# Kernel tuning notes

Hardware: AMD Instinct MI355X
Metric: run time of the kernel (lower is better)

## Reference

```python
import jax, jax.numpy as jnp
import numpy as np

NG, NT, E = 2500, 20000, 640000
SRC_DIM, DST_DIM, HID, OUT, NCLS = 128, 500, 128, 128, 16


def setup_inputs() -> dict:
    key = jax.random.key(0)
    ks = jax.random.split(key, 11)
    d = {
        "gene_feats": jax.random.normal(ks[0], (NG, SRC_DIM), jnp.float32),
        "train_feats": jax.random.normal(ks[1], (NT, DST_DIM), jnp.float32),
        "edge_src": jax.random.randint(ks[2], (E,), 0, NG),
        "edge_dst": jax.random.randint(ks[3], (E,), 0, NT),
        # conv1: SAGEConv((src_dim, dst_dim) -> hidden)
        "W1_neigh": jax.random.normal(ks[4], (SRC_DIM, HID), jnp.float32) / np.sqrt(SRC_DIM),
        "W1_self": jax.random.normal(ks[5], (DST_DIM, HID), jnp.float32) / np.sqrt(DST_DIM),
        "b1": jnp.zeros((HID,), jnp.float32),
        # conv2: SAGEConv(hidden -> out); src input is the raw gene features
        "W2_neigh": jax.random.normal(ks[6], (HID, OUT), jnp.float32) / np.sqrt(HID),
        "W2_self": jax.random.normal(ks[7], (HID, OUT), jnp.float32) / np.sqrt(HID),
        "b2": jnp.zeros((OUT,), jnp.float32),
        # classifier MLP
        "Wc1": jax.random.normal(ks[8], (OUT, OUT), jnp.float32) / np.sqrt(OUT),
        "bc1": jnp.zeros((OUT,), jnp.float32),
        "Wc2": jax.random.normal(ks[9], (OUT, NCLS), jnp.float32) / np.sqrt(OUT),
        "bc2": jnp.zeros((NCLS,), jnp.float32),
    }
    return d


def _segment_mean(msgs, dst, num_segments):
    # mean over in-edges; isolated dst nodes get 0 (DGL convention)
    sums = jax.ops.segment_sum(msgs, dst, num_segments=num_segments)
    cnt = jax.ops.segment_sum(jnp.ones((msgs.shape[0],), msgs.dtype), dst,
                              num_segments=num_segments)
    return sums / jnp.maximum(cnt, 1.0)[:, None]


def reference(gene_feats, train_feats, edge_src, edge_dst,
              W1_neigh, W1_self, b1, W2_neigh, W2_self, b2,
              Wc1, bc1, Wc2, bc2):
    # mean-aggregate gene (src) features onto train (dst) nodes
    agg = _segment_mean(gene_feats[edge_src], edge_dst, NT)  # [NT, SRC_DIM]
    # conv1: fc_self(h_dst) + fc_neigh(mean_neigh) + bias, then ReLU
    h1 = jax.nn.relu(train_feats @ W1_self + agg @ W1_neigh + b1)  # [NT, HID]
    # conv2 reuses raw gene features as src -> same mean aggregation
    h2 = jax.nn.relu(h1 @ W2_self + agg @ W2_neigh + b2)  # [NT, OUT]
    # classifier: Linear -> ReLU -> Linear
    return jax.nn.relu(h2 @ Wc1 + bc1) @ Wc2 + bc2  # [NT, NCLS]
```

## Files before the change

### kernel.cpp

```cpp
#include <hip/hip_runtime.h>


#define NG 2500
#define NT 20000
#define NE 640000
#define NCLS 16
#define CAP8 40
#define NTILE 1250

typedef unsigned short u16;
typedef unsigned int u32;

typedef float f32x4 __attribute__((ext_vector_type(4)));
typedef __bf16 bf16x8 __attribute__((ext_vector_type(8)));

__device__ __forceinline__ float b2f(u16 u) { return __uint_as_float(((u32)u) << 16); }
__device__ __forceinline__ float blo(u32 p) { return __uint_as_float(p << 16); }
__device__ __forceinline__ float bhi(u32 p) { return __uint_as_float(p & 0xffff0000u); }
__device__ __forceinline__ u16 f2b(float f) {
    u32 u = __float_as_uint(f);
    return (u16)((u + 0x7fffu + ((u >> 16) & 1u)) >> 16);
}

#define B1N 81920
#define B2N 32768
#define B3N 16384
#define B4N 2048
#define NEB 2500
#define CVB NTILE
#define GNB 625
#define PKB 520

__global__ __launch_bounds__(256) void k_prep(
    const int* __restrict__ esrc, const int* __restrict__ edst,
    int* __restrict__ cnt8, u16* __restrict__ csr8,
    const float* __restrict__ train, const float* __restrict__ gene,
    u16* __restrict__ AF, u32* __restrict__ GH32,
    const float* __restrict__ W1n, const float* __restrict__ W1s,
    const float* __restrict__ W2n, const float* __restrict__ W2s,
    const float* __restrict__ Wc1, const float* __restrict__ Wc2,
    u16* __restrict__ B1h, u16* __restrict__ B1l,
    u16* __restrict__ B2h, u16* __restrict__ B2l,
    u16* __restrict__ B3h, u16* __restrict__ B3l,
    u16* __restrict__ B4h, u16* __restrict__ B4l) {
    int blk = blockIdx.x, t = threadIdx.x;
    if (blk < NEB) {
        int xcc = __builtin_amdgcn_s_getreg(63508) & 7;
        int* mycnt = cnt8 + (size_t)xcc * NT;
        u16* mycsr = csr8 + (size_t)xcc * NT * CAP8;
        int e = blk * 256 + t;
        if (e < NE) {
            unsigned d = (unsigned)edst[e];
            if (d < NT) {
                int slot = atomicAdd(&mycnt[d], 1);
                if (slot < CAP8) mycsr[(size_t)d * CAP8 + slot] = (u16)esrc[e];
            }
        }
        return;
    }
    if (blk < NEB + CVB) {
        __shared__ __align__(16) u16 L[16 * 520];
        u32* L32 = (u32*)L;
        int tile = blk - NEB;
        for (int i = t; i < 160; i += 256) {
            int r = i / 10, c = i - r * 10;
            L32[r * 260 + 250 + c] = 0;
        }
        for (int i = t; i < 2000; i += 256) {
            int r = i / 125, c4 = i - r * 125;
            float4 v = *(const float4*)(train + (size_t)(tile * 16 + r) * 500 + c4 * 4);
            int base = r * 260 + c4 * 2;
            L32[base] = (u32)f2b(v.x) | ((u32)f2b(v.y) << 16);
            L32[base + 1] = (u32)f2b(v.z) | ((u32)f2b(v.w) << 16);
        }
        __syncthreads();
#pragma unroll
        for (int it = 0; it < 4; ++it) {
            int slot = t + it * 256;
            int kk = slot >> 6, lane = slot & 63;
            int m = lane & 15, q = lane >> 4;
            uint4 v = *(const uint4*)(L + m * 520 + kk * 32 + q * 8);
            *(uint4*)(AF + (((size_t)tile * 16 + kk) * 64 + lane) * 8) = v;
        }
        return;
    }
    if (blk < NEB + CVB + GNB) {
        int idx = (blk - NEB - CVB) * 256 + t;
        float2 v = ((const float2*)gene)[idx];
        GH32[idx] = (u32)f2b(v.x) | ((u32)f2b(v.y) << 16);
        return;
    }
    int idx = (blk - NEB - CVB - GNB) * 256 + t;
    float v = 0.f;
    u16 *ph = 0, *pl = 0;
    int off = 0;
    if (idx < B1N) {
        int j = idx & 7, l = (idx >> 3) & 63, rest = idx >> 9;
        int g = rest & 7, kk = rest >> 3;
        int k = kk * 32 + ((l >> 4) << 3) + j, n = (g << 4) + (l & 15);
        if (k < 500) v = W1s[k * 128 + n];
        else if (k >= 512) v = W1n[(k - 512) * 128 + n];
        ph = B1h; pl = B1l; off = idx;
    } else if (idx < B1N + B2N) {
        int e = idx - B1N;
        int j = e & 7, l = (e >> 3) & 63, rest = e >> 9;
        int g = rest & 7, kk = rest >> 3;
        int k = kk * 32 + ((l >> 4) << 3) + j, n = (g << 4) + (l & 15);
        v = (k < 128) ? W2s[k * 128 + n] : W2n[(k - 128) * 128 + n];
        ph = B2h; pl = B2l; off = e;
    } else if (idx < B1N + B2N + B3N) {
        int e = idx - (B1N + B2N);
        int j = e & 7, l = (e >> 3) & 63, rest = e >> 9;
        int g = rest & 7, kk = rest >> 3;
        int k = kk * 32 + ((l >> 4) << 3) + j, n = (g << 4) + (l & 15);
        v = Wc1[k * 128 + n];
        ph = B3h; pl = B3l; off = e;
    } else if (idx < B1N + B2N + B3N + B4N) {
        int e = idx - (B1N + B2N + B3N);
        int j = e & 7, l = (e >> 3) & 63, kk = e >> 9;
        int k = kk * 32 + ((l >> 4) << 3) + j, n = l & 15;
        v = Wc2[k * 16 + n];
        ph = B4h; pl = B4l; off = e;
    }
    if (ph) {
        u16 hi = f2b(v);
        u16 lo = f2b(v - b2f(hi));
        ph[off] = hi;
        pl[off] = lo;
    }
}

__global__ __launch_bounds__(512) void k_mega(
    const int* __restrict__ cnt8, const u16* __restrict__ csr8,
    const u16* __restrict__ GH, const u16* __restrict__ AF,
    const u16* __restrict__ B1h, const u16* __restrict__ B1l,
    const u16* __restrict__ B2h, const u16* __restrict__ B2l,
    const u16* __restrict__ B3h, const u16* __restrict__ B3l,
    const u16* __restrict__ B4h, const u16* __restrict__ B4l,
    const float* __restrict__ b1, const float* __restrict__ b2,
    const float* __restrict__ bc1, const float* __restrict__ bc2,
    float* __restrict__ out) {
    __shared__ __align__(16) u16 SAGh[32 * 136];
    __shared__ __align__(16) u16 S1h[32 * 136];
    __shared__ __align__(16) u16 S2h[32 * 136];
    int t = threadIdx.x;
    int row0 = blockIdx.x * 32;

    {
        int r = t >> 4, cg = t & 15;
        int d = row0 + r;
        float a[8];
#pragma unroll
        for (int p = 0; p < 8; ++p) a[p] = 0.f;
        int ctot = 0;
#pragma unroll
        for (int x = 0; x < 8; ++x) {
            int craw = cnt8[(size_t)x * NT + d];
            ctot += craw;
            int c = craw > CAP8 ? CAP8 : craw;
            const u16* crow = csr8 + ((size_t)x * NT + d) * CAP8;
            int j = 0;
            for (; j + 1 < c; j += 2) {
                int s0 = crow[j], s1 = crow[j + 1];
                uint4 p0 = *(const uint4*)(GH + (size_t)s0 * 128 + cg * 8);
                uint4 p1 = *(const uint4*)(GH + (size_t)s1 * 128 + cg * 8);
                a[0] += blo(p0.x); a[1] += bhi(p0.x);
                a[2] += blo(p0.y); a[3] += bhi(p0.y);
                a[4] += blo(p0.z); a[5] += bhi(p0.z);
                a[6] += blo(p0.w); a[7] += bhi(p0.w);
                a[0] += blo(p1.x); a[1] += bhi(p1.x);
                a[2] += blo(p1.y); a[3] += bhi(p1.y);
                a[4] += blo(p1.z); a[5] += bhi(p1.z);
                a[6] += blo(p1.w); a[7] += bhi(p1.w);
            }
            if (j < c) {
                int s = crow[j];
                uint4 p0 = *(const uint4*)(GH + (size_t)s * 128 + cg * 8);
                a[0] += blo(p0.x); a[1] += bhi(p0.x);
                a[2] += blo(p0.y); a[3] += bhi(p0.y);
                a[4] += blo(p0.z); a[5] += bhi(p0.z);
                a[6] += blo(p0.w); a[7] += bhi(p0.w);
            }
        }
        float inv = (ctot > 0) ? 1.f / (float)ctot : 0.f;
        int base = (r * 136 + cg * 8) >> 1;
        u32* SH = (u32*)SAGh;
#pragma unroll
        for (int p = 0; p < 4; ++p) {
            float x = a[2 * p] * inv, y = a[2 * p + 1] * inv;
            SH[base + p] = (u32)f2b(x) | ((u32)f2b(y) << 16);
        }
    }
    __syncthreads();

    int lane = t & 63, g = t >> 6;
    int m = lane & 15, q = lane >> 4, n16 = lane & 15;
    size_t tile0 = (size_t)blockIdx.x * 2;

    const u16* aB0 = AF + ((tile0 * 16) * 64 + lane) * 8;
    const u16* aB1 = AF + (((tile0 + 1) * 16) * 64 + lane) * 8;
    int hr0 = m * 136 + q * 8;
    int hr1 = (16 + m) * 136 + q * 8;
    int cr0 = q * 4, cr1 = 16 + q * 4;
    const f32x4 z4 = {0.f, 0.f, 0.f, 0.f};
    f32x4 acc0 = z4, acc1 = z4;

#pragma unroll 4
    for (int kk = 0; kk < 16; ++kk) {
        bf16x8 a0 = *(const bf16x8*)(aB0 + kk * 512);
        bf16x8 a1 = *(const bf16x8*)(aB1 + kk * 512);
        size_t bo = ((size_t)(kk * 8 + g) * 64 + lane) * 8;
        bf16x8 bh = *(const bf16x8*)(B1h + bo);
        bf16x8 bl = *(const bf16x8*)(B1l + bo);
        acc0 = __builtin_amdgcn_mfma_f32_16x16x32_bf16(a0, bh, acc0, 0, 0, 0);
        acc0 = __builtin_amdgcn_mfma_f32_16x16x32_bf16(a0, bl, acc0, 0, 0, 0);
        acc1 = __builtin_amdgcn_mfma_f32_16x16x32_bf16(a1, bh, acc1, 0, 0, 0);
        acc1 = __builtin_amdgcn_mfma_f32_16x16x32_bf16(a1, bl, acc1, 0, 0, 0);
    }
#pragma unroll
    for (int kk = 16; kk < 20; ++kk) {
        int o = (kk - 16) * 32;
        bf16x8 ah0 = *(const bf16x8*)(SAGh + hr0 + o);
        bf16x8 ah1 = *(const bf16x8*)(SAGh + hr1 + o);
        size_t bo = ((size_t)(kk * 8 + g) * 64 + lane) * 8;
        bf16x8 bh = *(const bf16x8*)(B1h + bo);
        bf16x8 bl = *(const bf16x8*)(B1l + bo);
        acc0 = __builtin_amdgcn_mfma_f32_16x16x32_bf16(ah0, bh, acc0, 0, 0, 0);
        acc0 = __builtin_amdgcn_mfma_f32_16x16x32_bf16(ah0, bl, acc0, 0, 0, 0);
        acc1 = __builtin_amdgcn_mfma_f32_16x16x32_bf16(ah1, bh, acc1, 0, 0, 0);
        acc1 = __builtin_amdgcn_mfma_f32_16x16x32_bf16(ah1, bl, acc1, 0, 0, 0);
    }
    {
        int n = g * 16 + n16;
        float bias = b1[n];
#pragma unroll
        for (int rg = 0; rg < 4; ++rg) {
            float v0 = acc0[rg] + bias; v0 = v0 > 0.f ? v0 : 0.f;
            float v1 = acc1[rg] + bias; v1 = v1 > 0.f ? v1 : 0.f;
            S1h[(cr0 + rg) * 136 + n] = f2b(v0);
            S1h[(cr1 + rg) * 136 + n] = f2b(v1);
        }
    }
    __syncthreads();

    acc0 = z4; acc1 = z4;
#pragma unroll
    for (int kk = 0; kk < 8; ++kk) {
        const u16* Ph = (kk < 4) ? S1h : SAGh;
        int o = (kk & 3) * 32;
        bf16x8 ah0 = *(const bf16x8*)(Ph + hr0 + o);
        bf16x8 ah1 = *(const bf16x8*)(Ph + hr1 + o);
        size_t bo = ((size_t)(kk * 8 + g) * 64 + lane) * 8;
        bf16x8 bh = *(const bf16x8*)(B2h + bo);
        bf16x8 bl = *(const bf16x8*)(B2l + bo);
        acc0 = __builtin_amdgcn_mfma_f32_16x16x32_bf16(ah0, bh, acc0, 0, 0, 0);
        acc0 = __builtin_amdgcn_mfma_f32_16x16x32_bf16(ah0, bl, acc0, 0, 0, 0);
        acc1 = __builtin_amdgcn_mfma_f32_16x16x32_bf16(ah1, bh, acc1, 0, 0, 0);
        acc1 = __builtin_amdgcn_mfma_f32_16x16x32_bf16(ah1, bl, acc1, 0, 0, 0);
    }
    {
        int n = g * 16 + n16;
        float bias = b2[n];
#pragma unroll
        for (int rg = 0; rg < 4; ++rg) {
            float v0 = acc0[rg] + bias; v0 = v0 > 0.f ? v0 : 0.f;
            float v1 = acc1[rg] + bias; v1 = v1 > 0.f ? v1 : 0.f;
            S2h[(cr0 + rg) * 136 + n] = f2b(v0);
            S2h[(cr1 + rg) * 136 + n] = f2b(v1);
        }
    }
    __syncthreads();

    acc0 = z4; acc1 = z4;
#pragma unroll
    for (int kk = 0; kk < 4; ++kk) {
        int o = kk * 32;
        bf16x8 ah0 = *(const bf16x8*)(S2h + hr0 + o);
        bf16x8 ah1 = *(const bf16x8*)(S2h + hr1 + o);
        size_t bo = ((size_t)(kk * 8 + g) * 64 + lane) * 8;
        bf16x8 bh = *(const bf16x8*)(B3h + bo);
        bf16x8 bl = *(const bf16x8*)(B3l + bo);
        acc0 = __builtin_amdgcn_mfma_f32_16x16x32_bf16(ah0, bh, acc0, 0, 0, 0);
        acc0 = __builtin_amdgcn_mfma_f32_16x16x32_bf16(ah0, bl, acc0, 0, 0, 0);
        acc1 = __builtin_amdgcn_mfma_f32_16x16x32_bf16(ah1, bh, acc1, 0, 0, 0);
        acc1 = __builtin_amdgcn_mfma_f32_16x16x32_bf16(ah1, bl, acc1, 0, 0, 0);
    }
    {
        int n = g * 16 + n16;
        float bias = bc1[n];
#pragma unroll
        for (int rg = 0; rg < 4; ++rg) {
            float v0 = acc0[rg] + bias; v0 = v0 > 0.f ? v0 : 0.f;
            float v1 = acc1[rg] + bias; v1 = v1 > 0.f ? v1 : 0.f;
            S1h[(cr0 + rg) * 136 + n] = f2b(v0);
            S1h[(cr1 + rg) * 136 + n] = f2b(v1);
        }
    }
    __syncthreads();

    if (g < 2) {
        int hr = (g == 0) ? hr0 : hr1;
        int cr = (g == 0) ? cr0 : cr1;
        f32x4 a4 = z4;
#pragma unroll
        for (int kk = 0; kk < 4; ++kk) {
            bf16x8 ah = *(const bf16x8*)(S1h + hr + kk * 32);
            size_t bo = ((size_t)kk * 64 + lane) * 8;
            bf16x8 bh = *(const bf16x8*)(B4h + bo);
            bf16x8 bl = *(const bf16x8*)(B4l + bo);
            a4 = __builtin_amdgcn_mfma_f32_16x16x32_bf16(ah, bh, a4, 0, 0, 0);
            a4 = __builtin_amdgcn_mfma_f32_16x16x32_bf16(ah, bl, a4, 0, 0, 0);
        }
        float bias = bc2[n16];
#pragma unroll
        for (int rg = 0; rg < 4; ++rg)
            out[(size_t)(row0 + cr + rg) * NCLS + n16] = a4[rg] + bias;
    }
}

extern "C" void kernel_launch(void* const* d_in, const int* in_sizes, int n_in,
                              void* d_out, int out_size, void* d_ws, size_t ws_size,
                              hipStream_t stream) {
    const float* gene = (const float*)d_in[0];
    const float* train = (const float*)d_in[1];
    const int* esrc = (const int*)d_in[2];
    const int* edst = (const int*)d_in[3];

    char* ws = (char*)d_ws;
    int* cnt8 = (int*)(ws + 0);
    u16* csr8 = (u16*)(ws + 640000);
    u16* AF = (u16*)(ws + 13440000);
    u16* GH = (u16*)(ws + 33920000);
    u16* B1h = (u16*)(ws + 34560000);
    u16* B1l = (u16*)(ws + 34723840);
    u16* B2h = (u16*)(ws + 34887680);
    u16* B2l = (u16*)(ws + 34953216);
    u16* B3h = (u16*)(ws + 35018752);
    u16* B3l = (u16*)(ws + 35051520);
    u16* B4h = (u16*)(ws + 35084288);
    u16* B4l = (u16*)(ws + 35088384);

    hipMemsetAsync(cnt8, 0, 8 * NT * sizeof(int), stream);
    k_prep<<<NEB + CVB + GNB + PKB, 256, 0, stream>>>(
        esrc, edst, cnt8, csr8, train, gene, AF, (u32*)GH,
        (const float*)d_in[4], (const float*)d_in[5], (const float*)d_in[7],
        (const float*)d_in[8], (const float*)d_in[10], (const float*)d_in[12],
        B1h, B1l, B2h, B2l, B3h, B3l, B4h, B4l);
    k_mega<<<NT / 32, 512, 0, stream>>>(
        cnt8, csr8, GH, AF, B1h, B1l, B2h, B2l, B3h, B3l, B4h, B4l,
        (const float*)d_in[6], (const float*)d_in[9], (const float*)d_in[11],
        (const float*)d_in[13], (float*)d_out);
}
```

Before: 185.3 us.

## Remap row tiles across XCDs and restructure neighbor gather to wave-per-row

The fused SAGE kernel now assigns each block two non-adjacent 16-row tiles through a permutation. The apparent aim is to spread neighbouring tiles across the chip's L2 partitions. The neighbour-mean gather changes from 16 threads per row with 16-byte loads to one wavefront per row, where each lane loads one 32-bit packed bf16 pair; each wave handles four rows in turn. The per-bucket CSR capacity shrinks from 40 to 32, which reduces workspace and scan footprint but drops more edges if any bucket overflows.

```diff
diff --git a/kernel.cpp b/kernel.cpp
--- a/kernel.cpp
+++ b/kernel.cpp
@@ -5,7 +5,7 @@
 #define NT 20000
 #define NE 640000
 #define NCLS 16
-#define CAP8 40
+#define CAP8 32
 #define NTILE 1250
 
 typedef unsigned short u16;
@@ -144,64 +144,65 @@
     __shared__ __align__(16) u16 S1h[32 * 136];
     __shared__ __align__(16) u16 S2h[32 * 136];
     int t = threadIdx.x;
-    int row0 = blockIdx.x * 32;
+    int lane = t & 63, w = t >> 6;
+
+    int b = blockIdx.x;
+    int t0, t1;
+    if (b < 616) {
+        int k = (b + 4) & 7;
+        int j = (b >> 3) * 2;
+        t0 = k + 8 * j;
+        t1 = t0 + 8;
+    } else {
+        t0 = 1232 + 2 * (b - 616);
+        t1 = t0 + 1;
+    }
+    int grow0 = t0 * 16, grow1 = t1 * 16;
+    const u32* GH32 = (const u32*)GH;
 
     {
-        int r = t >> 4, cg = t & 15;
-        int d = row0 + r;
-        float a[8];
-#pragma unroll
-        for (int p = 0; p < 8; ++p) a[p] = 0.f;
-        int ctot = 0;
-#pragma unroll
-        for (int x = 0; x < 8; ++x) {
-            int craw = cnt8[(size_t)x * NT + d];
-            ctot += craw;
-            int c = craw > CAP8 ? CAP8 : craw;
-            const u16* crow = csr8 + ((size_t)x * NT + d) * CAP8;
-            int j = 0;
-            for (; j + 1 < c; j += 2) {
-                int s0 = crow[j], s1 = crow[j + 1];
-                uint4 p0 = *(const uint4*)(GH + (size_t)s0 * 128 + cg * 8);
-                uint4 p1 = *(const uint4*)(GH + (size_t)s1 * 128 + cg * 8);
-                a[0] += blo(p0.x); a[1] += bhi(p0.x);
-                a[2] += blo(p0.y); a[3] += bhi(p0.y);
-                a[4] += blo(p0.z); a[5] += bhi(p0.z);
-                a[6] += blo(p0.w); a[7] += bhi(p0.w);
-                a[0] += blo(p1.x); a[1] += bhi(p1.x);
-                a[2] += blo(p1.y); a[3] += bhi(p1.y);
-                a[4] += blo(p1.z); a[5] += bhi(p1.z);
-                a[6] += blo(p1.w); a[7] += bhi(p1.w);
+        u32* SH = (u32*)SAGh;
+#pragma unroll
+        for (int i = 0; i < 4; ++i) {
+            int r = w * 4 + i;
+            int d = (r < 16) ? grow0 + r : grow1 + (r - 16);
+            float a0 = 0.f, a1 = 0.f;
+            int ctot = 0;
+            for (int x = 0; x < 8; ++x) {
+                int craw = cnt8[x * NT + d];
+                ctot += craw;
+                int c = craw > CAP8 ? CAP8 : craw;
+                const u16* crow = csr8 + ((size_t)x * NT + d) * CAP8;
+                int j = 0;
+                for (; j + 1 < c; j += 2) {
+                    int s0 = crow[j], s1 = crow[j + 1];
+                    u32 p0 = GH32[s0 * 64 + lane];
+                    u32 p1 = GH32[s1 * 64 + lane];
+                    a0 += blo(p0) + blo(p1);
+                    a1 += bhi(p0) + bhi(p1);
+                }
+                if (j < c) {
+                    int s = crow[j];
+                    u32 p = GH32[s * 64 + lane];
+                    a0 += blo(p);
+                    a1 += bhi(p);
+                }
             }
-            if (j < c) {
-                int s = crow[j];
-                uint4 p0 = *(const uint4*)(GH + (size_t)s * 128 + cg * 8);
-                a[0] += blo(p0.x); a[1] += bhi(p0.x);
-                a[2] += blo(p0.y); a[3] += bhi(p0.y);
-                a[4] += blo(p0.z); a[5] += bhi(p0.z);
-                a[6] += blo(p0.w); a[7] += bhi(p0.w);
-            }
-        }
-        float inv = (ctot > 0) ? 1.f / (float)ctot : 0.f;
-        int base = (r * 136 + cg * 8) >> 1;
-        u32* SH = (u32*)SAGh;
-#pragma unroll
-        for (int p = 0; p < 4; ++p) {
-            float x = a[2 * p] * inv, y = a[2 * p + 1] * inv;
-            SH[base + p] = (u32)f2b(x) | ((u32)f2b(y) << 16);
+            float inv = (ctot > 0) ? 1.f / (float)ctot : 0.f;
+            a0 *= inv; a1 *= inv;
+            SH[r * 68 + lane] = (u32)f2b(a0) | ((u32)f2b(a1) << 16);
         }
     }
     __syncthreads();
 
-    int lane = t & 63, g = t >> 6;
+    int g = w;
     int m = lane & 15, q = lane >> 4, n16 = lane & 15;
-    size_t tile0 = (size_t)blockIdx.x * 2;
-
-    const u16* aB0 = AF + ((tile0 * 16) * 64 + lane) * 8;
-    const u16* aB1 = AF + (((tile0 + 1) * 16) * 64 + lane) * 8;
+
+    const u16* aB0 = AF + (((size_t)t0 * 16) * 64 + lane) * 8;
+    const u16* aB1 = AF + (((size_t)t1 * 16) * 64 + lane) * 8;
     int hr0 = m * 136 + q * 8;
     int hr1 = (16 + m) * 136 + q * 8;
-    int cr0 = q * 4, cr1 = 16 + q * 4;
+    int cr0 = q * 4;
     const f32x4 z4 = {0.f, 0.f, 0.f, 0.f};
     f32x4 acc0 = z4, acc1 = z4;
 
@@ -238,7 +239,7 @@
             float v0 = acc0[rg] + bias; v0 = v0 > 0.f ? v0 : 0.f;
             float v1 = acc1[rg] + bias; v1 = v1 > 0.f ? v1 : 0.f;
             S1h[(cr0 + rg) * 136 + n] = f2b(v0);
-            S1h[(cr1 + rg) * 136 + n] = f2b(v1);
+            S1h[(16 + cr0 + rg) * 136 + n] = f2b(v1);
         }
     }
     __syncthreads();
@@ -266,7 +267,7 @@
             float v0 = acc0[rg] + bias; v0 = v0 > 0.f ? v0 : 0.f;
             float v1 = acc1[rg] + bias; v1 = v1 > 0.f ? v1 : 0.f;
             S2h[(cr0 + rg) * 136 + n] = f2b(v0);
-            S2h[(cr1 + rg) * 136 + n] = f2b(v1);
+            S2h[(16 + cr0 + rg) * 136 + n] = f2b(v1);
         }
     }
     __syncthreads();
@@ -293,14 +294,14 @@
             float v0 = acc0[rg] + bias; v0 = v0 > 0.f ? v0 : 0.f;
             float v1 = acc1[rg] + bias; v1 = v1 > 0.f ? v1 : 0.f;
             S1h[(cr0 + rg) * 136 + n] = f2b(v0);
-            S1h[(cr1 + rg) * 136 + n] = f2b(v1);
+            S1h[(16 + cr0 + rg) * 136 + n] = f2b(v1);
         }
     }
     __syncthreads();
 
     if (g < 2) {
         int hr = (g == 0) ? hr0 : hr1;
-        int cr = (g == 0) ? cr0 : cr1;
+        int growx = (g == 0) ? grow0 : grow1;
         f32x4 a4 = z4;
 #pragma unroll
         for (int kk = 0; kk < 4; ++kk) {
@@ -314,7 +315,7 @@
         float bias = bc2[n16];
 #pragma unroll
         for (int rg = 0; rg < 4; ++rg)
-            out[(size_t)(row0 + cr + rg) * NCLS + n16] = a4[rg] + bias;
+            out[(size_t)(growx + cr0 + rg) * NCLS + n16] = a4[rg] + bias;
     }
 }
 
@@ -329,16 +330,16 @@
     char* ws = (char*)d_ws;
     int* cnt8 = (int*)(ws + 0);
     u16* csr8 = (u16*)(ws + 640000);
-    u16* AF = (u16*)(ws + 13440000);
-    u16* GH = (u16*)(ws + 33920000);
-    u16* B1h = (u16*)(ws + 34560000);
-    u16* B1l = (u16*)(ws + 34723840);
-    u16* B2h = (u16*)(ws + 34887680);
-    u16* B2l = (u16*)(ws + 34953216);
-    u16* B3h = (u16*)(ws + 35018752);
-    u16* B3l = (u16*)(ws + 35051520);
-    u16* B4h = (u16*)(ws + 35084288);
-    u16* B4l = (u16*)(ws + 35088384);
+    u16* AF = (u16*)(ws + 10880000);
+    u16* GH = (u16*)(ws + 31360000);
+    u16* B1h = (u16*)(ws + 32000000);
+    u16* B1l = (u16*)(ws + 32163840);
+    u16* B2h = (u16*)(ws + 32327680);
+    u16* B2l = (u16*)(ws + 32393216);
+    u16* B3h = (u16*)(ws + 32458752);
+    u16* B3l = (u16*)(ws + 32491520);
+    u16* B4h = (u16*)(ws + 32524288);
+    u16* B4l = (u16*)(ws + 32528384);
 
     hipMemsetAsync(cnt8, 0, 8 * NT * sizeof(int), stream);
     k_prep<<<NEB + CVB + GNB + PKB, 256, 0, stream>>>(
@@ -346,7 +347,7 @@
         (const float*)d_in[4], (const float*)d_in[5], (const float*)d_in[7],
         (const float*)d_in[8], (const float*)d_in[10], (const float*)d_in[12],
         B1h, B1l, B2h, B2l, B3h, B3l, B4h, B4l);
-    k_mega<<<NT / 32, 512, 0, stream>>>(
+    k_mega<<<625, 512, 0, stream>>>(
         cnt8, csr8, GH, AF, B1h, B1l, B2h, B2l, B3h, B3l, B4h, B4l,
         (const float*)d_in[6], (const float*)d_in[9], (const float*)d_in[11],
         (const float*)d_in[13], (float*)d_out);
```

New measurement: 202.8 us. 1.09x slower.
